# Optimization experiments

Measured on AMD Instinct MI355X. Metric: run time of the kernel, lower is better.

Reference implementation:

```python
import jax, jax.numpy as jnp
import numpy as np

B, N, D = 8, 256, 16   # batch, set size, in_dim
HID = 256              # hidden width (hidden_dims[:-1])
H = 128                # attention feature dim (hidden_dims[-1])
DH = 64                # per-dim feature dim d_h
NH = 4                 # attention heads


def _made_masks():
    in_deg = np.arange(1, D + 1)
    h_deg = (np.arange(HID) % (D - 1)) + 1
    out_deg = np.repeat(in_deg, H)  # per-dim contiguous layout -> reshape(..., D, H)
    m0 = h_deg[None, :] >= in_deg[:, None]
    m1 = h_deg[None, :] >= h_deg[:, None]
    m2 = out_deg[None, :] > h_deg[:, None]
    return jnp.array(m0), jnp.array(m1), jnp.array(m2)


def setup_inputs() -> dict:
    key = jax.random.key(0)
    ks = iter(jax.random.split(key, 40))
    def w(fi, fo):
        return jax.random.normal(next(ks), (fi, fo), jnp.float32) / np.sqrt(fi)
    inp = {"t": jnp.array([0.5], jnp.float32),
           "x": jax.random.normal(next(ks), (B, N, D), jnp.float32)}
    qd = [D, HID, HID, H * D]
    kd = [D, HID, HID, H]
    dd = [DH + 2, HID, HID, H, 1]
    for i in range(3):
        inp[f"q_w{i}"] = w(qd[i], qd[i + 1]); inp[f"q_b{i}"] = jnp.zeros((qd[i + 1],), jnp.float32)
        inp[f"k_w{i}"] = w(kd[i], kd[i + 1]); inp[f"k_b{i}"] = jnp.zeros((kd[i + 1],), jnp.float32)
        inp[f"v_w{i}"] = w(kd[i], kd[i + 1]); inp[f"v_b{i}"] = jnp.zeros((kd[i + 1],), jnp.float32)
    inp["p_w"] = w(H, DH); inp["p_b"] = jnp.zeros((DH,), jnp.float32)
    for i in range(4):
        inp[f"d_w{i}"] = w(dd[i], dd[i + 1]); inp[f"d_b{i}"] = jnp.zeros((dd[i + 1],), jnp.float32)
    inp["q_m0"], inp["q_m1"], inp["q_m2"] = _made_masks()
    return inp


def reference(t, x, q_w0, q_b0, k_w0, k_b0, v_w0, v_b0, q_w1, q_b1, k_w1, k_b1, v_w1, v_b1,
              q_w2, q_b2, k_w2, k_b2, v_w2, v_b2, p_w, p_b,
              d_w0, d_b0, d_w1, d_b1, d_w2, d_b2, d_w3, d_b3, q_m0, q_m1, q_m2):
    # --- exclusive net: MADE query (hollow per dim), MLP key/value, diagonal-masked attention ---
    hq = jax.nn.relu(x @ (q_w0 * q_m0) + q_b0)
    hq = jax.nn.relu(hq @ (q_w1 * q_m1) + q_b1)
    q = (hq @ (q_w2 * q_m2) + q_b2).reshape(B, N, D, H)      # [B,N,D,H]

    def mlp3(z, w0, b0, w1, b1, w2, b2):
        z = jnp.tanh(z @ w0 + b0)
        z = jnp.tanh(z @ w1 + b1)
        return z @ w2 + b2

    k = mlp3(x, k_w0, k_b0, k_w1, k_b1, k_w2, k_b2)          # [B,N,H] (shared across dims)
    v = mlp3(x, v_w0, v_b0, v_w1, v_b1, v_w2, v_b2)          # [B,N,H]

    dh = H // NH
    qh = q.transpose(0, 2, 1, 3).reshape(B, D, N, NH, dh).transpose(0, 1, 3, 2, 4)  # [B,D,NH,N,dh]
    kh = k.reshape(B, N, NH, dh).transpose(0, 2, 1, 3)        # [B,NH,N,dh]
    vh = v.reshape(B, N, NH, dh).transpose(0, 2, 1, 3)

    # einsum avoids materializing the repeat_interleaved key/value (same math)
    scores = jnp.einsum('bdhnc,bhmc->bdhnm', qh, kh) / np.sqrt(dh)
    scores = jnp.where(jnp.eye(N, dtype=bool), -jnp.inf, scores)  # mask self-attention (hollow)
    att = jax.nn.softmax(scores, axis=-1)
    o = jnp.einsum('bdhnm,bhmc->bdhnc', att, vh)              # [B,D,NH,N,dh]
    o = o.transpose(0, 1, 3, 2, 4).reshape(B, D, N, H).transpose(0, 2, 1, 3)  # [B,N,D,H]
    hfeat = o @ p_w + p_b                                     # [B,N,D,DH], hollow wrt x[...,d]

    # --- dimwise net: y_d = MLP([t, x_d, h_d]); exact diagonal Jacobian via jvp on x channel ---
    tb = jnp.broadcast_to(t.reshape(()), (B, N, D, 1)).astype(x.dtype)
    def dimwise(xc):
        z = jnp.concatenate([tb, xc, hfeat], -1)              # [B,N,D,2+DH]
        z = jnp.tanh(z @ d_w0 + d_b0)
        z = jnp.tanh(z @ d_w1 + d_b1)
        z = jnp.tanh(z @ d_w2 + d_b2)
        return (z @ d_w3 + d_b3)[..., 0]                      # [B,N,D]

    y, jac = jax.jvp(dimwise, (x[..., None],), (jnp.ones((B, N, D, 1), x.dtype),))
    return y, jac
```

## Files before the change

kernel.cpp:

```cpp
#include <hip/hip_runtime.h>
#include <hip/hip_bf16.h>

constexpr int kB = 8, kN = 256, kD = 16, kHID = 256, kH = 128, kDH = 64, kdh = 32;
constexpr int kBN = kB * kN;
constexpr int kP  = kBN * kD;

__device__ __forceinline__ float b2f(__hip_bfloat16 v) { return __bfloat162float(v); }
__device__ __forceinline__ __hip_bfloat16 f2b(float v) { return __float2bfloat16(v); }
__device__ __forceinline__ unsigned short f2bs(float v) {
    __hip_bfloat16 h = __float2bfloat16(v);
    return *(unsigned short*)&h;
}

__device__ __forceinline__ float tanh_fast(float v) {
    float e = __expf(2.f * v);
    return 1.f - 2.f * __builtin_amdgcn_rcpf(e + 1.f);
}

typedef short s8v  __attribute__((ext_vector_type(8)));
typedef float f4v  __attribute__((ext_vector_type(4)));
#define MFMA(a, b, c) __builtin_amdgcn_mfma_f32_16x16x32_bf16((a), (b), (c), 0, 0, 0)

__global__ __launch_bounds__(256) void prep_frag(
    const float* p_w, const float* d_w0, const float* d_w1, const float* d_w2,
    const float* k_w0, const float* k_w1, const float* k_w2,
    const float* v_w0, const float* v_w1, const float* v_w2,
    const float* q_w0, const float* q_w1, const float* q_w2,
    __hip_bfloat16* pwf, __hip_bfloat16* w0f, __hip_bfloat16* w1f, __hip_bfloat16* w2f,
    __hip_bfloat16* k0f, __hip_bfloat16* k1f, __hip_bfloat16* k2f,
    __hip_bfloat16* v0f, __hip_bfloat16* v1f, __hip_bfloat16* v2f,
    __hip_bfloat16* q0f, __hip_bfloat16* q1f, __hip_bfloat16* q2f)
{
    const int tile = blockIdx.x * 4 + (threadIdx.x >> 6);
    const int lane = threadIdx.x & 63;
    const float* src; __hip_bfloat16* dst; int N, NT, local, Kreal = 1 << 30, mask = 0;
    if (tile < 16)        { src = p_w;        dst = pwf; N = 64;   NT = 4;   local = tile; }
    else if (tile < 48)   { src = d_w0 + 512; dst = w0f; N = 256;  NT = 16;  local = tile - 16; }
    else if (tile < 176)  { src = d_w1;       dst = w1f; N = 256;  NT = 16;  local = tile - 48; }
    else if (tile < 240)  { src = d_w2;       dst = w2f; N = 128;  NT = 8;   local = tile - 176; }
    else if (tile < 256)  { src = k_w0;       dst = k0f; N = 256;  NT = 16;  local = tile - 240; Kreal = 16; }
    else if (tile < 272)  { src = v_w0;       dst = v0f; N = 256;  NT = 16;  local = tile - 256; Kreal = 16; }
    else if (tile < 288)  { src = q_w0;       dst = q0f; N = 256;  NT = 16;  local = tile - 272; Kreal = 16; mask = 1; }
    else if (tile < 416)  { src = k_w1;       dst = k1f; N = 256;  NT = 16;  local = tile - 288; }
    else if (tile < 544)  { src = v_w1;       dst = v1f; N = 256;  NT = 16;  local = tile - 416; }
    else if (tile < 672)  { src = q_w1;       dst = q1f; N = 256;  NT = 16;  local = tile - 544; mask = 2; }
    else if (tile < 736)  { src = k_w2;       dst = k2f; N = 128;  NT = 8;   local = tile - 672; }
    else if (tile < 800)  { src = v_w2;       dst = v2f; N = 128;  NT = 8;   local = tile - 736; }
    else                  { src = q_w2;       dst = q2f; N = 2048; NT = 128; local = tile - 800; mask = 3; }
    const int kt = local / NT, nt = local % NT;
    const int row0 = kt * 32 + (lane >> 4) * 8;
    const int col  = nt * 16 + (lane & 15);
    __hip_bfloat16* o = dst + ((size_t)local * 64 + lane) * 8;
    #pragma unroll
    for (int j = 0; j < 8; ++j) {
        const int r = row0 + j;
        float w = (r < Kreal) ? src[(size_t)r * N + col] : 0.f;
        if (mask == 1 && !((col % 15) >= r))        w = 0.f;
        if (mask == 2 && !((col % 15) >= (r % 15))) w = 0.f;
        if (mask == 3 && !((col >> 7) > (r % 15)))  w = 0.f;
        o[j] = f2b(w);
    }
}

__global__ __launch_bounds__(256) void mlp_kernel(
    const float* x,
    const float* k_b0, const float* k_b1, const float* k_b2,
    const float* v_b0, const float* v_b1, const float* v_b2,
    const float* q_b0, const float* q_b1,
    const __hip_bfloat16* k0f, const __hip_bfloat16* k1f, const __hip_bfloat16* k2f,
    const __hip_bfloat16* v0f, const __hip_bfloat16* v1f, const __hip_bfloat16* v2f,
    const __hip_bfloat16* q0f, const __hip_bfloat16* q1f,
    __hip_bfloat16* kbuf, __hip_bfloat16* vbuf, __hip_bfloat16* h1q)
{
    constexpr int SA = 264;
    constexpr int SX = 40;
    __shared__ __hip_bfloat16 xin[32 * SX];
    __shared__ __hip_bfloat16 bufA[32 * SA];
    __shared__ __hip_bfloat16 bufB[32 * SA];

    const int tid  = threadIdx.x;
    const int wv   = tid >> 6, lane = tid & 63;
    const int lx   = lane & 15, quad = lane >> 4;
    const int path = blockIdx.x >> 6;
    const int r0   = (blockIdx.x & 63) * 32;

    auto ldA = [&](const __hip_bfloat16* buf, int stride, int m0, int k0) -> s8v {
        return *(const s8v*)(buf + (m0 + lx) * stride + k0 + quad * 8);
    };
    auto ldB = [&](const __hip_bfloat16* wf, int NT, int kt, int nt) -> s8v {
        return *(const s8v*)(wf + (((size_t)(kt * NT + nt) * 64 + lane) << 3));
    };

    for (int idx = tid; idx < 1024; idx += 256) {
        const int row = idx >> 5, c = idx & 31;
        xin[row * SX + c] = f2b(c < 16 ? x[(r0 + row) * kD + c] : 0.f);
    }

    const __hip_bfloat16* F0[3] = { k0f, v0f, q0f };
    const __hip_bfloat16* F1[3] = { k1f, v1f, q1f };
    const __hip_bfloat16* F2[2] = { k2f, v2f };
    const float* Ba0[3] = { k_b0, v_b0, q_b0 };
    const float* Ba1[3] = { k_b1, v_b1, q_b1 };
    const float* Ba2[2] = { k_b2, v_b2 };
    __hip_bfloat16* O2[2] = { kbuf, vbuf };

    __syncthreads();

    {
        f4v acc[4][2] = {};
        const s8v a0 = ldA(xin, SX, 0, 0);
        const s8v a1 = ldA(xin, SX, 16, 0);
        #pragma unroll
        for (int j = 0; j < 4; ++j) {
            s8v b = ldB(F0[path], 16, 0, wv * 4 + j);
            acc[j][0] = MFMA(a0, b, acc[j][0]);
            acc[j][1] = MFMA(a1, b, acc[j][1]);
        }
        #pragma unroll
        for (int j = 0; j < 4; ++j) {
            const int n = (wv * 4 + j) * 16 + lx;
            const float bb = Ba0[path][n];
            #pragma unroll
            for (int mt = 0; mt < 2; ++mt)
            #pragma unroll
            for (int r = 0; r < 4; ++r) {
                const float v = acc[j][mt][r] + bb;
                const float z = (path == 2) ? fmaxf(v, 0.f) : tanh_fast(v);
                bufA[(mt * 16 + quad * 4 + r) * SA + n] = f2b(z);
            }
        }
    }
    __syncthreads();

    {
        f4v acc[4][2] = {};
        #pragma unroll
        for (int kt = 0; kt < 8; ++kt) {
            const s8v a0 = ldA(bufA, SA, 0, kt * 32);
            const s8v a1 = ldA(bufA, SA, 16, kt * 32);
            #pragma unroll
            for (int j = 0; j < 4; ++j) {
                s8v b = ldB(F1[path], 16, kt, wv * 4 + j);
                acc[j][0] = MFMA(a0, b, acc[j][0]);
                acc[j][1] = MFMA(a1, b, acc[j][1]);
            }
        }
        #pragma unroll
        for (int j = 0; j < 4; ++j) {
            const int n = (wv * 4 + j) * 16 + lx;
            const float bb = Ba1[path][n];
            #pragma unroll
            for (int mt = 0; mt < 2; ++mt)
            #pragma unroll
            for (int r = 0; r < 4; ++r) {
                const int m = mt * 16 + quad * 4 + r;
                const float v = acc[j][mt][r] + bb;
                if (path == 2) {
                    h1q[(size_t)(r0 + m) * 256 + n] = f2b(fmaxf(v, 0.f));
                } else {
                    bufB[m * SA + n] = f2b(tanh_fast(v));
                }
            }
        }
    }
    if (path == 2) return;
    __syncthreads();

    {
        f4v acc[2][2] = {};
        #pragma unroll
        for (int kt = 0; kt < 8; ++kt) {
            const s8v a0 = ldA(bufB, SA, 0, kt * 32);
            const s8v a1 = ldA(bufB, SA, 16, kt * 32);
            #pragma unroll
            for (int j = 0; j < 2; ++j) {
                s8v b = ldB(F2[path], 8, kt, wv * 2 + j);
                acc[j][0] = MFMA(a0, b, acc[j][0]);
                acc[j][1] = MFMA(a1, b, acc[j][1]);
            }
        }
        #pragma unroll
        for (int j = 0; j < 2; ++j) {
            const int n = (wv * 2 + j) * 16 + lx;
            const float bb = Ba2[path][n];
            #pragma unroll
            for (int mt = 0; mt < 2; ++mt)
            #pragma unroll
            for (int r = 0; r < 4; ++r) {
                const int m = mt * 16 + quad * 4 + r;
                O2[path][(size_t)(r0 + m) * kH + n] = f2b(acc[j][mt][r] + bb);
            }
        }
    }
}

__global__ __launch_bounds__(256) void qgemm_kernel(
    const float* q_b2, const __hip_bfloat16* h1q, const __hip_bfloat16* q2f,
    __hip_bfloat16* qbuf)
{
    constexpr int SA = 264;
    __shared__ __hip_bfloat16 hin[32 * SA];

    const int tid  = threadIdx.x;
    const int wv   = tid >> 6, lane = tid & 63;
    const int lx   = lane & 15, quad = lane >> 4;
    const int ct   = blockIdx.x & 7;
    const int r0   = (blockIdx.x >> 3) * 32;

    for (int idx = tid; idx < 1024; idx += 256) {
        const int row = idx >> 5, seg = idx & 31;
        *(f4v*)(hin + row * SA + seg * 8) = *(const f4v*)(h1q + (size_t)(r0 + row) * 256 + seg * 8);
    }
    __syncthreads();

    f4v acc[4][2] = {};
    #pragma unroll
    for (int kt = 0; kt < 8; ++kt) {
        const s8v a0 = *(const s8v*)(hin + lx * SA + kt * 32 + quad * 8);
        const s8v a1 = *(const s8v*)(hin + (16 + lx) * SA + kt * 32 + quad * 8);
        #pragma unroll
        for (int j = 0; j < 4; ++j) {
            s8v b = *(const s8v*)(q2f + (((size_t)(kt * 128 + ct * 16 + wv * 4 + j) * 64 + lane) << 3));
            acc[j][0] = MFMA(a0, b, acc[j][0]);
            acc[j][1] = MFMA(a1, b, acc[j][1]);
        }
    }
    const float scale = 0.17677669529663687f;
    #pragma unroll
    for (int j = 0; j < 4; ++j) {
        const int col = ct * 256 + (wv * 4 + j) * 16 + lx;
        const float bb = q_b2[col];
        #pragma unroll
        for (int mt = 0; mt < 2; ++mt)
        #pragma unroll
        for (int r = 0; r < 4; ++r) {
            const int row = r0 + mt * 16 + quad * 4 + r;
            qbuf[(size_t)row * 2048 + col] = f2b((acc[j][mt][r] + bb) * scale);
        }
    }
}

__global__ __launch_bounds__(256, 2) void attn_kernel(
    const __hip_bfloat16* qbuf, const __hip_bfloat16* kbuf, const __hip_bfloat16* vbuf,
    __hip_bfloat16* obuf)
{
    constexpr int SP = 264;
    __shared__ short Pl[4][16 * SP];

    const int blk = blockIdx.x;
    const int hd = blk & 3;
    const int d  = (blk >> 2) & 15;
    const int b  = blk >> 6;

    const int wv   = threadIdx.x >> 6;
    const int lane = threadIdx.x & 63;
    const int lx = lane & 15, quad = lane >> 4;
    short* Pw = &Pl[wv][0];

    const short* kb = (const short*)kbuf;
    const short* vb = (const short*)vbuf;
    const short* qb = (const short*)qbuf;

    s8v kfrag[16];
    #pragma unroll
    for (int mt = 0; mt < 16; ++mt)
        kfrag[mt] = *(const s8v*)(kb + (size_t)(b * 256 + mt * 16 + lx) * 128 + hd * 32 + quad * 8);

    s8v vfrag[2][8];
    #pragma unroll
    for (int ntv = 0; ntv < 2; ++ntv)
    #pragma unroll
    for (int kt = 0; kt < 8; ++kt) {
        s8v v;
        #pragma unroll
        for (int j = 0; j < 8; ++j)
            v[j] = vb[(size_t)(b * 256 + kt * 32 + quad * 8 + j) * 128 + hd * 32 + ntv * 16 + lx];
        vfrag[ntv][kt] = v;
    }

    const float LOG2E = 1.4426950408889634f;

    for (int mi = 0; mi < 4; ++mi) {
        const int q0 = wv * 64 + mi * 16;

        s8v qfrag = *(const s8v*)(qb + (size_t)(b * 256 + q0 + lx) * 2048 + d * 128 + hd * 32 + quad * 8);

        f4v acc[16];
        #pragma unroll
        for (int mt = 0; mt < 16; ++mt) acc[mt] = f4v{0.f, 0.f, 0.f, 0.f};
        #pragma unroll
        for (int mt = 0; mt < 16; ++mt) acc[mt] = MFMA(kfrag[mt], qfrag, acc[mt]);

        const int qg = q0 + lx;
        float mx = -3.0e38f;
        #pragma unroll
        for (int mt = 0; mt < 16; ++mt)
        #pragma unroll
        for (int r = 0; r < 4; ++r) {
            const int key = mt * 16 + quad * 4 + r;
            float s = (key == qg) ? -3.0e38f : acc[mt][r];
            acc[mt][r] = s;
            mx = fmaxf(mx, s);
        }
        mx = fmaxf(mx, __shfl_xor(mx, 16, 64));
        mx = fmaxf(mx, __shfl_xor(mx, 32, 64));

        const float nmxc = -mx * LOG2E;
        float l = 0.f;
        #pragma unroll
        for (int mt = 0; mt < 16; ++mt)
        #pragma unroll
        for (int r = 0; r < 4; ++r) {
            float p = exp2f(__builtin_fmaf(acc[mt][r], LOG2E, nmxc));
            acc[mt][r] = p;
            l += p;
        }
        l += __shfl_xor(l, 16, 64);
        l += __shfl_xor(l, 32, 64);

        #pragma unroll
        for (int mt = 0; mt < 16; ++mt) {
            unsigned short h0 = f2bs(acc[mt][0]);
            unsigned short h1 = f2bs(acc[mt][1]);
            unsigned short h2 = f2bs(acc[mt][2]);
            unsigned short h3 = f2bs(acc[mt][3]);
            uint2 w;
            w.x = (unsigned int)h0 | ((unsigned int)h1 << 16);
            w.y = (unsigned int)h2 | ((unsigned int)h3 << 16);
            *(uint2*)(Pw + lx * SP + mt * 16 + quad * 4) = w;
        }
        __asm__ volatile("s_waitcnt lgkmcnt(0)" ::: "memory");

        f4v av[2] = { f4v{0.f,0.f,0.f,0.f}, f4v{0.f,0.f,0.f,0.f} };
        #pragma unroll
        for (int kt = 0; kt < 8; ++kt) {
            s8v a = *(const s8v*)(Pw + lx * SP + kt * 32 + quad * 8);
            av[0] = MFMA(a, vfrag[0][kt], av[0]);
            av[1] = MFMA(a, vfrag[1][kt], av[1]);
        }
        __asm__ volatile("s_waitcnt lgkmcnt(0)" ::: "memory");

        #pragma unroll
        for (int r = 0; r < 4; ++r) {
            const float lr = __shfl(l, quad * 4 + r, 64);
            const float inv = __builtin_amdgcn_rcpf(lr);
            const int qrow = q0 + quad * 4 + r;
            #pragma unroll
            for (int ntv = 0; ntv < 2; ++ntv) {
                obuf[((size_t)((b * 256 + qrow) * 16 + d)) * 128 + hd * 32 + ntv * 16 + lx]
                    = f2b(av[ntv][r] * inv);
            }
        }
    }
}

__global__ __launch_bounds__(256) void dim_kernel(
    const float* t, const float* x,
    const float* p_b, const float* d_w0, const float* d_b0,
    const float* d_b1, const float* d_b2, const float* d_w3, const float* d_b3,
    const __hip_bfloat16* pwf, const __hip_bfloat16* w0f,
    const __hip_bfloat16* w1f, const __hip_bfloat16* w2f,
    const __hip_bfloat16* obuf, float* out)
{
    constexpr int SA = 264;
    constexpr int SO = 136;
    constexpr int SH = 72;
    __shared__ __hip_bfloat16 bufA[32 * SA];
    __shared__ __hip_bfloat16 bufB[32 * SA];
    __shared__ __hip_bfloat16 bufH[16 * SH];
    __shared__ float xvs[16];

    const int tid  = threadIdx.x;
    const int wv   = tid >> 6, lane = tid & 63;
    const int lx   = lane & 15, quad = lane >> 4;
    const int p0   = blockIdx.x * 16;
    const float tval = t[0];

    auto ldA = [&](const __hip_bfloat16* buf, int stride, int m0, int k0) -> s8v {
        return *(const s8v*)(buf + (m0 + lx) * stride + k0 + quad * 8);
    };
    auto ldBf = [&](const __hip_bfloat16* wf, int NT, int kt, int nt) -> s8v {
        return *(const s8v*)(wf + (((size_t)(kt * NT + nt) * 64 + lane) << 3));
    };

    for (int idx = tid; idx < 256; idx += 256) {
        const int row = idx >> 4, ch = idx & 15;
        *(f4v*)(bufA + row * SO + ch * 8) = *(const f4v*)(obuf + (size_t)(p0 + row) * kH + ch * 8);
    }
    if (tid < 16) xvs[tid] = x[p0 + tid];
    __syncthreads();

    {
        f4v acc0 = {};
        #pragma unroll
        for (int ktile = 0; ktile < 4; ++ktile) {
            s8v b  = ldBf(pwf, 4, ktile, wv);
            s8v a0 = ldA(bufA, SO, 0, ktile * 32);
            acc0 = MFMA(a0, b, acc0);
        }
        const int n = wv * 16 + lx;
        const float bb = p_b[n];
        #pragma unroll
        for (int r = 0; r < 4; ++r)
            bufH[(quad * 4 + r) * SH + n] = f2b(acc0[r] + bb);
    }
    __syncthreads();

    {
        f4v acc[4] = {};
        #pragma unroll
        for (int ktile = 0; ktile < 2; ++ktile) {
            s8v a0 = ldA(bufH, SH, 0, ktile * 32);
            #pragma unroll
            for (int j = 0; j < 4; ++j) {
                s8v b = ldBf(w0f, 16, ktile, wv * 4 + j);
                acc[j] = MFMA(a0, b, acc[j]);
            }
        }
        #pragma unroll
        for (int j = 0; j < 4; ++j) {
            const int n = (wv * 4 + j) * 16 + lx;
            const float base = d_b0[n] + tval * d_w0[n];
            const float wx   = d_w0[256 + n];
            #pragma unroll
            for (int r = 0; r < 4; ++r) {
                const int m = quad * 4 + r;
                const float z = tanh_fast(acc[j][r] + base + xvs[m] * wx);
                bufB[m * SA + n]        = f2b(z);
                bufB[(m + 16) * SA + n] = f2b((1.f - z * z) * wx);
            }
        }
    }
    __syncthreads();

    {
        f4v acc[4][2] = {};
        #pragma unroll
        for (int ktile = 0; ktile < 8; ++ktile) {
            s8v a0 = ldA(bufB, SA, 0,  ktile * 32);
            s8v a1 = ldA(bufB, SA, 16, ktile * 32);
            #pragma unroll
            for (int j = 0; j < 4; ++j) {
                s8v b = ldBf(w1f, 16, ktile, wv * 4 + j);
                acc[j][0] = MFMA(a0, b, acc[j][0]);
                acc[j][1] = MFMA(a1, b, acc[j][1]);
            }
        }
        #pragma unroll
        for (int j = 0; j < 4; ++j) {
            const int n = (wv * 4 + j) * 16 + lx;
            const float b1 = d_b1[n];
            #pragma unroll
            for (int r = 0; r < 4; ++r) {
                const int m = quad * 4 + r;
                const float z  = tanh_fast(acc[j][0][r] + b1);
                const float zd = (1.f - z * z) * acc[j][1][r];
                bufA[m * SA + n]        = f2b(z);
                bufA[(m + 16) * SA + n] = f2b(zd);
            }
        }
    }
    __syncthreads();

    {
        f4v acc[2][2] = {};
        #pragma unroll
        for (int ktile = 0; ktile < 8; ++ktile) {
            s8v a0 = ldA(bufA, SA, 0,  ktile * 32);
            s8v a1 = ldA(bufA, SA, 16, ktile * 32);
            #pragma unroll
            for (int j = 0; j < 2; ++j) {
                s8v b = ldBf(w2f, 8, ktile, wv * 2 + j);
                acc[j][0] = MFMA(a0, b, acc[j][0]);
                acc[j][1] = MFMA(a1, b, acc[j][1]);
            }
        }
        #pragma unroll
        for (int j = 0; j < 2; ++j) {
            const int n = (wv * 2 + j) * 16 + lx;
            const float b2 = d_b2[n];
            #pragma unroll
            for (int r = 0; r < 4; ++r) {
                const int m = quad * 4 + r;
                const float z  = tanh_fast(acc[j][0][r] + b2);
                const float zd = (1.f - z * z) * acc[j][1][r];
                bufB[m * SO + n]        = f2b(z);
                bufB[(m + 16) * SO + n] = f2b(zd);
            }
        }
    }
    __syncthreads();

    {
        const int p = tid >> 4, s = tid & 15;
        float yv = 0.f, jv = 0.f;
        #pragma unroll
        for (int i = 0; i < 8; ++i) {
            const int n = s + i * 16;
            const float w = d_w3[n];
            yv += b2f(bufB[p * SO + n]) * w;
            jv += b2f(bufB[(p + 16) * SO + n]) * w;
        }
        #pragma unroll
        for (int off = 8; off > 0; off >>= 1) {
            yv += __shfl_down(yv, off, 16);
            jv += __shfl_down(jv, off, 16);
        }
        if (s == 0) {
            out[p0 + p]      = yv + d_b3[0];
            out[kP + p0 + p] = jv;
        }
    }
}

extern "C" void kernel_launch(void* const* d_in, const int* in_sizes, int n_in,
                              void* d_out, int out_size, void* d_ws, size_t ws_size,
                              hipStream_t stream)
{
    typedef const float* fp;
    fp t    = (fp)d_in[0];
    fp x    = (fp)d_in[1];
    fp q_w0 = (fp)d_in[2],  q_b0 = (fp)d_in[3];
    fp k_w0 = (fp)d_in[4],  k_b0 = (fp)d_in[5];
    fp v_w0 = (fp)d_in[6],  v_b0 = (fp)d_in[7];
    fp q_w1 = (fp)d_in[8],  q_b1 = (fp)d_in[9];
    fp k_w1 = (fp)d_in[10], k_b1 = (fp)d_in[11];
    fp v_w1 = (fp)d_in[12], v_b1 = (fp)d_in[13];
    fp q_w2 = (fp)d_in[14], q_b2 = (fp)d_in[15];
    fp k_w2 = (fp)d_in[16], k_b2 = (fp)d_in[17];
    fp v_w2 = (fp)d_in[18], v_b2 = (fp)d_in[19];
    fp p_w  = (fp)d_in[20], p_b  = (fp)d_in[21];
    fp d_w0 = (fp)d_in[22], d_b0 = (fp)d_in[23];
    fp d_w1 = (fp)d_in[24], d_b1 = (fp)d_in[25];
    fp d_w2 = (fp)d_in[26], d_b2 = (fp)d_in[27];
    fp d_w3 = (fp)d_in[28], d_b3 = (fp)d_in[29];

    __hip_bfloat16* wsb  = (__hip_bfloat16*)d_ws;
    __hip_bfloat16* kbuf = wsb;
    __hip_bfloat16* vbuf = kbuf + (size_t)kBN * kH;
    __hip_bfloat16* qbuf = vbuf + (size_t)kBN * kH;
    __hip_bfloat16* obuf = qbuf + (size_t)kBN * kD * kH;
    __hip_bfloat16* pwf  = obuf + (size_t)kP * kH;
    __hip_bfloat16* w0f  = pwf + 8192;
    __hip_bfloat16* w1f  = w0f + 16384;
    __hip_bfloat16* w2f  = w1f + 65536;
    __hip_bfloat16* k0f  = w2f + 32768;
    __hip_bfloat16* v0f  = k0f + 8192;
    __hip_bfloat16* q0f  = v0f + 8192;
    __hip_bfloat16* k1f  = q0f + 8192;
    __hip_bfloat16* v1f  = k1f + 65536;
    __hip_bfloat16* q1f  = v1f + 65536;
    __hip_bfloat16* k2f  = q1f + 65536;
    __hip_bfloat16* v2f  = k2f + 32768;
    __hip_bfloat16* q2f  = v2f + 32768;
    __hip_bfloat16* h1q  = q2f + 524288;

    float* out = (float*)d_out;

    prep_frag<<<456, 256, 0, stream>>>(p_w, d_w0, d_w1, d_w2,
        k_w0, k_w1, k_w2, v_w0, v_w1, v_w2, q_w0, q_w1, q_w2,
        pwf, w0f, w1f, w2f, k0f, k1f, k2f, v0f, v1f, v2f, q0f, q1f, q2f);
    mlp_kernel<<<192, 256, 0, stream>>>(x,
        k_b0, k_b1, k_b2, v_b0, v_b1, v_b2, q_b0, q_b1,
        k0f, k1f, k2f, v0f, v1f, v2f, q0f, q1f, kbuf, vbuf, h1q);
    qgemm_kernel<<<(kBN / 32) * 8, 256, 0, stream>>>(q_b2, h1q, q2f, qbuf);
    attn_kernel<<<kB * kD * 4, 256, 0, stream>>>(qbuf, kbuf, vbuf, obuf);
    dim_kernel<<<kP / 16, 256, 0, stream>>>(t, x, p_b, d_w0, d_b0, d_b1, d_b2, d_w3, d_b3,
        pwf, w0f, w1f, w2f, obuf, out);
}
```

Baseline: 193.0 us.

## Fuse query projection GEMM into attention kernel and pre-fragment K/V layouts

Removes the separate qgemm kernel. Each attention block now computes its own 256x32 query slice from the hidden activations and stores it in shared memory, so the 8 MB bf16 query buffer is never written to or read back from global memory. The MLP kernel now writes h1q, K and V directly in MFMA fragment order, so the attention kernel loads them as contiguous 16-byte vectors instead of strided scalar gathers. The cost is extra shared memory in the attention kernel, which may lower occupancy, plus redundant reads of h1q across the 4 head blocks.

```diff
diff --git a/kernel.cpp b/kernel.cpp
--- a/kernel.cpp
+++ b/kernel.cpp
@@ -70,7 +70,7 @@
     const __hip_bfloat16* k0f, const __hip_bfloat16* k1f, const __hip_bfloat16* k2f,
     const __hip_bfloat16* v0f, const __hip_bfloat16* v1f, const __hip_bfloat16* v2f,
     const __hip_bfloat16* q0f, const __hip_bfloat16* q1f,
-    __hip_bfloat16* kbuf, __hip_bfloat16* vbuf, __hip_bfloat16* h1q)
+    __hip_bfloat16* kbufF, __hip_bfloat16* vbufF, __hip_bfloat16* h1qF)
 {
     constexpr int SA = 264;
     constexpr int SX = 40;
@@ -102,7 +102,6 @@
     const float* Ba0[3] = { k_b0, v_b0, q_b0 };
     const float* Ba1[3] = { k_b1, v_b1, q_b1 };
     const float* Ba2[2] = { k_b2, v_b2 };
-    __hip_bfloat16* O2[2] = { kbuf, vbuf };
 
     __syncthreads();
 
@@ -156,7 +155,10 @@
                 const int m = mt * 16 + quad * 4 + r;
                 const float v = acc[j][mt][r] + bb;
                 if (path == 2) {
-                    h1q[(size_t)(r0 + m) * 256 + n] = f2b(fmaxf(v, 0.f));
+                    const int kt2 = (wv * 4 + j) >> 1;
+                    const int q2  = ((wv * 4 + j) & 1) * 2 + (lx >> 3);
+                    h1qF[(size_t)(((r0 >> 4) + mt) * 8 + kt2) * 512
+                         + (q2 * 16 + quad * 4 + r) * 8 + (lx & 7)] = f2b(fmaxf(v, 0.f));
                 } else {
                     bufB[m * SA + n] = f2b(tanh_fast(v));
                 }
@@ -179,73 +181,42 @@
                 acc[j][1] = MFMA(a1, b, acc[j][1]);
             }
         }
+        const int bidx = r0 >> 8;
+        const int ktv  = (r0 >> 5) & 7;
         #pragma unroll
         for (int j = 0; j < 2; ++j) {
-            const int n = (wv * 2 + j) * 16 + lx;
+            const int n  = (wv * 2 + j) * 16 + lx;
             const float bb = Ba2[path][n];
+            const int hd = n >> 5;
             #pragma unroll
             for (int mt = 0; mt < 2; ++mt)
             #pragma unroll
             for (int r = 0; r < 4; ++r) {
-                const int m = mt * 16 + quad * 4 + r;
-                O2[path][(size_t)(r0 + m) * kH + n] = f2b(acc[j][mt][r] + bb);
-            }
-        }
-    }
-}
-
-__global__ __launch_bounds__(256) void qgemm_kernel(
-    const float* q_b2, const __hip_bfloat16* h1q, const __hip_bfloat16* q2f,
-    __hip_bfloat16* qbuf)
-{
-    constexpr int SA = 264;
-    __shared__ __hip_bfloat16 hin[32 * SA];
-
-    const int tid  = threadIdx.x;
-    const int wv   = tid >> 6, lane = tid & 63;
-    const int lx   = lane & 15, quad = lane >> 4;
-    const int ct   = blockIdx.x & 7;
-    const int r0   = (blockIdx.x >> 3) * 32;
-
-    for (int idx = tid; idx < 1024; idx += 256) {
-        const int row = idx >> 5, seg = idx & 31;
-        *(f4v*)(hin + row * SA + seg * 8) = *(const f4v*)(h1q + (size_t)(r0 + row) * 256 + seg * 8);
-    }
-    __syncthreads();
-
-    f4v acc[4][2] = {};
-    #pragma unroll
-    for (int kt = 0; kt < 8; ++kt) {
-        const s8v a0 = *(const s8v*)(hin + lx * SA + kt * 32 + quad * 8);
-        const s8v a1 = *(const s8v*)(hin + (16 + lx) * SA + kt * 32 + quad * 8);
-        #pragma unroll
-        for (int j = 0; j < 4; ++j) {
-            s8v b = *(const s8v*)(q2f + (((size_t)(kt * 128 + ct * 16 + wv * 4 + j) * 64 + lane) << 3));
-            acc[j][0] = MFMA(a0, b, acc[j][0]);
-            acc[j][1] = MFMA(a1, b, acc[j][1]);
-        }
-    }
-    const float scale = 0.17677669529663687f;
-    #pragma unroll
-    for (int j = 0; j < 4; ++j) {
-        const int col = ct * 256 + (wv * 4 + j) * 16 + lx;
-        const float bb = q_b2[col];
-        #pragma unroll
-        for (int mt = 0; mt < 2; ++mt)
-        #pragma unroll
-        for (int r = 0; r < 4; ++r) {
-            const int row = r0 + mt * 16 + quad * 4 + r;
-            qbuf[(size_t)row * 2048 + col] = f2b((acc[j][mt][r] + bb) * scale);
+                const int gr = r0 + mt * 16 + quad * 4 + r;
+                const __hip_bfloat16 hv = f2b(acc[j][mt][r] + bb);
+                if (path == 0) {
+                    const int mtg = (gr >> 4) & 15;
+                    kbufF[(size_t)(((bidx * 4 + hd) * 16 + mtg) * 64
+                          + ((n & 31) >> 3) * 16 + (gr & 15)) * 8 + (lx & 7)] = hv;
+                } else {
+                    const int m5 = gr & 31;
+                    vbufF[(size_t)((((bidx * 4 + hd) * 2 + ((n >> 4) & 1)) * 8 + ktv) * 64
+                          + (m5 >> 3) * 16 + lx) * 8 + (m5 & 7)] = hv;
+                }
+            }
         }
     }
 }
 
 __global__ __launch_bounds__(256, 2) void attn_kernel(
-    const __hip_bfloat16* qbuf, const __hip_bfloat16* kbuf, const __hip_bfloat16* vbuf,
+    const float* q_b2, const __hip_bfloat16* h1qF, const __hip_bfloat16* q2f,
+    const __hip_bfloat16* kbufF, const __hip_bfloat16* vbufF,
     __hip_bfloat16* obuf)
 {
     constexpr int SP = 264;
+    constexpr int QP = 40;
     __shared__ short Pl[4][16 * SP];
+    __shared__ short Qw[256 * QP];
 
     const int blk = blockIdx.x;
     const int hd = blk & 3;
@@ -257,33 +228,57 @@
     const int lx = lane & 15, quad = lane >> 4;
     short* Pw = &Pl[wv][0];
 
-    const short* kb = (const short*)kbuf;
-    const short* vb = (const short*)vbuf;
-    const short* qb = (const short*)qbuf;
+    const short* hq = (const short*)h1qF;
+    const short* kb = (const short*)kbufF;
+    const short* vb = (const short*)vbufF;
+    const int bh = b * 4 + hd;
+
+    f4v qacc[4][2] = {};
+    #pragma unroll
+    for (int kt = 0; kt < 8; ++kt) {
+        const s8v b0 = *(const s8v*)(q2f + (((size_t)(kt * 128 + d * 8 + hd * 2 + 0) * 64 + lane) << 3));
+        const s8v b1 = *(const s8v*)(q2f + (((size_t)(kt * 128 + d * 8 + hd * 2 + 1) * 64 + lane) << 3));
+        #pragma unroll
+        for (int mt = 0; mt < 4; ++mt) {
+            const s8v a = *(const s8v*)(hq + ((size_t)((b * 16 + wv * 4 + mt) * 8 + kt) * 512 + lane * 8));
+            qacc[mt][0] = MFMA(a, b0, qacc[mt][0]);
+            qacc[mt][1] = MFMA(a, b1, qacc[mt][1]);
+        }
+    }
 
     s8v kfrag[16];
     #pragma unroll
     for (int mt = 0; mt < 16; ++mt)
-        kfrag[mt] = *(const s8v*)(kb + (size_t)(b * 256 + mt * 16 + lx) * 128 + hd * 32 + quad * 8);
-
+        kfrag[mt] = *(const s8v*)(kb + ((size_t)(bh * 16 + mt) * 64 + lane) * 8);
     s8v vfrag[2][8];
     #pragma unroll
     for (int ntv = 0; ntv < 2; ++ntv)
     #pragma unroll
-    for (int kt = 0; kt < 8; ++kt) {
-        s8v v;
-        #pragma unroll
-        for (int j = 0; j < 8; ++j)
-            v[j] = vb[(size_t)(b * 256 + kt * 32 + quad * 8 + j) * 128 + hd * 32 + ntv * 16 + lx];
-        vfrag[ntv][kt] = v;
-    }
+    for (int kt = 0; kt < 8; ++kt)
+        vfrag[ntv][kt] = *(const s8v*)(vb + ((size_t)((bh * 2 + ntv) * 8 + kt) * 64 + lane) * 8);
+
+    {
+        const float scale = 0.17677669529663687f;
+        #pragma unroll
+        for (int jn = 0; jn < 2; ++jn) {
+            const float bb = q_b2[d * 128 + hd * 32 + jn * 16 + lx];
+            #pragma unroll
+            for (int mt = 0; mt < 4; ++mt)
+            #pragma unroll
+            for (int r = 0; r < 4; ++r) {
+                const int lrow = wv * 64 + mt * 16 + quad * 4 + r;
+                Qw[lrow * QP + jn * 16 + lx] = (short)f2bs((qacc[mt][jn][r] + bb) * scale);
+            }
+        }
+    }
+    __syncthreads();
 
     const float LOG2E = 1.4426950408889634f;
 
     for (int mi = 0; mi < 4; ++mi) {
         const int q0 = wv * 64 + mi * 16;
 
-        s8v qfrag = *(const s8v*)(qb + (size_t)(b * 256 + q0 + lx) * 2048 + d * 128 + hd * 32 + quad * 8);
+        const s8v qfrag = *(const s8v*)(Qw + (q0 + lx) * QP + quad * 8);
 
         f4v acc[16];
         #pragma unroll
@@ -535,25 +530,24 @@
     fp d_w2 = (fp)d_in[26], d_b2 = (fp)d_in[27];
     fp d_w3 = (fp)d_in[28], d_b3 = (fp)d_in[29];
 
-    __hip_bfloat16* wsb  = (__hip_bfloat16*)d_ws;
-    __hip_bfloat16* kbuf = wsb;
-    __hip_bfloat16* vbuf = kbuf + (size_t)kBN * kH;
-    __hip_bfloat16* qbuf = vbuf + (size_t)kBN * kH;
-    __hip_bfloat16* obuf = qbuf + (size_t)kBN * kD * kH;
-    __hip_bfloat16* pwf  = obuf + (size_t)kP * kH;
-    __hip_bfloat16* w0f  = pwf + 8192;
-    __hip_bfloat16* w1f  = w0f + 16384;
-    __hip_bfloat16* w2f  = w1f + 65536;
-    __hip_bfloat16* k0f  = w2f + 32768;
-    __hip_bfloat16* v0f  = k0f + 8192;
-    __hip_bfloat16* q0f  = v0f + 8192;
-    __hip_bfloat16* k1f  = q0f + 8192;
-    __hip_bfloat16* v1f  = k1f + 65536;
-    __hip_bfloat16* q1f  = v1f + 65536;
-    __hip_bfloat16* k2f  = q1f + 65536;
-    __hip_bfloat16* v2f  = k2f + 32768;
-    __hip_bfloat16* q2f  = v2f + 32768;
-    __hip_bfloat16* h1q  = q2f + 524288;
+    __hip_bfloat16* wsb   = (__hip_bfloat16*)d_ws;
+    __hip_bfloat16* kbufF = wsb;
+    __hip_bfloat16* vbufF = kbufF + (size_t)kBN * kH;
+    __hip_bfloat16* obuf  = vbufF + (size_t)kBN * kH;
+    __hip_bfloat16* pwf   = obuf + (size_t)kP * kH;
+    __hip_bfloat16* w0f   = pwf + 8192;
+    __hip_bfloat16* w1f   = w0f + 16384;
+    __hip_bfloat16* w2f   = w1f + 65536;
+    __hip_bfloat16* k0f   = w2f + 32768;
+    __hip_bfloat16* v0f   = k0f + 8192;
+    __hip_bfloat16* q0f   = v0f + 8192;
+    __hip_bfloat16* k1f   = q0f + 8192;
+    __hip_bfloat16* v1f   = k1f + 65536;
+    __hip_bfloat16* q1f   = v1f + 65536;
+    __hip_bfloat16* k2f   = q1f + 65536;
+    __hip_bfloat16* v2f   = k2f + 32768;
+    __hip_bfloat16* q2f   = v2f + 32768;
+    __hip_bfloat16* h1qF  = q2f + 524288;
 
     float* out = (float*)d_out;
 
@@ -562,9 +556,8 @@
         pwf, w0f, w1f, w2f, k0f, k1f, k2f, v0f, v1f, v2f, q0f, q1f, q2f);
     mlp_kernel<<<192, 256, 0, stream>>>(x,
         k_b0, k_b1, k_b2, v_b0, v_b1, v_b2, q_b0, q_b1,
-        k0f, k1f, k2f, v0f, v1f, v2f, q0f, q1f, kbuf, vbuf, h1q);
-    qgemm_kernel<<<(kBN / 32) * 8, 256, 0, stream>>>(q_b2, h1q, q2f, qbuf);
-    attn_kernel<<<kB * kD * 4, 256, 0, stream>>>(qbuf, kbuf, vbuf, obuf);
+        k0f, k1f, k2f, v0f, v1f, v2f, q0f, q1f, kbufF, vbufF, h1qF);
+    attn_kernel<<<kB * kD * 4, 256, 0, stream>>>(q_b2, h1qF, q2f, kbufF, vbufF, obuf);
     dim_kernel<<<kP / 16, 256, 0, stream>>>(t, x, p_b, d_w0, d_b0, d_b1, d_b2, d_w3, d_b3,
         pwf, w0f, w1f, w2f, obuf, out);
 }
```

Result: no change. 189.4 us, median of 2 (-1.8%).
